# Kernel tuning notes

Hardware: AMD Instinct MI355X
Metric: run time of the kernel (lower is better)

The kernel has to match this reference:

```python
import jax, jax.numpy as jnp
import numpy as np

VOCAB, VEC, HID, ATT, DOM, B, S = 50000, 300, 256, 500, 16, 64, 128


def _gru_scan(gi_all, h0, Whh, bhh):
    # gi_all: [S,B,3H] precomputed input projections; returns hs: [S,B,H]
    def step(h, gi):
        gh = h @ Whh.T + bhh
        i_r, i_z, i_n = jnp.split(gi, 3, axis=-1)
        h_r, h_z, h_n = jnp.split(gh, 3, axis=-1)
        r = jax.nn.sigmoid(i_r + h_r)
        zg = jax.nn.sigmoid(i_z + h_z)
        n = jnp.tanh(i_n + r * h_n)
        h_new = (1.0 - zg) * n + zg * h
        return h_new, h_new
    _, hs = jax.lax.scan(step, h0, gi_all)
    return hs


def setup_inputs() -> dict:
    key = jax.random.key(0)
    ks = jax.random.split(key, 16)
    def xavier(k, shape):
        fan_in, fan_out = shape[-1], shape[0]
        std = float(np.sqrt(2.0 / (fan_in + fan_out)))
        return jax.random.normal(k, shape, dtype=jnp.float32) * std
    inp = {
        'x': jax.random.randint(ks[0], (B, S), 0, VOCAB),
        'z': jax.random.randint(ks[1], (B,), 0, DOM),
        'emb': jax.random.normal(ks[2], (VOCAB, VEC), dtype=jnp.float32) * 0.1,
        'Wih_f': xavier(ks[3], (3 * HID, VEC)),
        'Whh_f': xavier(ks[4], (3 * HID, HID)),
        'bih_f': jnp.zeros((3 * HID,), jnp.float32),
        'bhh_f': jnp.zeros((3 * HID,), jnp.float32),
        'Wih_b': xavier(ks[5], (3 * HID, VEC)),
        'Whh_b': xavier(ks[6], (3 * HID, HID)),
        'bih_b': jnp.zeros((3 * HID,), jnp.float32),
        'bhh_b': jnp.zeros((3 * HID,), jnp.float32),
        'att_fc_W': xavier(ks[7], (ATT, 2 * HID)),
        'att_fc_b': jnp.zeros((ATT,), jnp.float32),
        'att_weight': xavier(ks[8], (DOM, ATT)),
        'fc_W': xavier(ks[9], (2, 2 * HID)),
        'fc_b': jnp.zeros((2,), jnp.float32),
    }
    return inp


def reference(x, z, emb, Wih_f, Whh_f, bih_f, bhh_f, Wih_b, Whh_b, bih_b, bhh_b,
              att_fc_W, att_fc_b, att_weight, fc_W, fc_b):
    xe = emb[x]                              # [B,S,VEC]
    xs = jnp.transpose(xe, (1, 0, 2))        # [S,B,VEC] (seq-major like torch GRU)
    h0 = jnp.zeros((x.shape[0], HID), jnp.float32)
    gi_f = jnp.einsum('sbv,gv->sbg', xs, Wih_f) + bih_f
    hs_f = _gru_scan(gi_f, h0, Whh_f, bhh_f)                       # [S,B,H]
    gi_b = jnp.einsum('sbv,gv->sbg', xs[::-1], Wih_b) + bih_b
    hs_b = _gru_scan(gi_b, h0, Whh_b, bhh_b)[::-1]                 # [S,B,H]
    h = jnp.transpose(jnp.concatenate([hs_f, hs_b], axis=-1), (1, 0, 2))  # [B,S,2H]
    hr = jnp.tanh(jnp.einsum('bsh,ah->bsa', h, att_fc_W) + att_fc_b)      # [B,S,ATT]
    # batched gather of per-domain attention vector, then per-row dot
    u = jnp.einsum('bsa,ba->bs', hr, att_weight[z])                        # [B,S]
    att = jax.nn.softmax(u, axis=1)                                        # [B,S]
    pooled = jnp.einsum('bsh,bs->bh', h, att)                              # [B,2H]
    # dropout is identity in eval mode
    return pooled @ fc_W.T + fc_b                                          # [B,2]
```

## Files before the change

kernel.cpp:

```cpp
#include <hip/hip_runtime.h>
#include <math.h>

#define VEC   300
#define HID   256
#define ATT   500
#define NB    64
#define NS    128
#define G3    768
#define GIC   1536
#define H2    512

typedef _Float16 half1;
typedef _Float16 h2_t  __attribute__((ext_vector_type(2)));
typedef _Float16 f16x8 __attribute__((ext_vector_type(8)));
typedef float    f32x4 __attribute__((ext_vector_type(4)));

struct __align__(16) H8 { h2_t a, b, c, d; };

#if __has_builtin(__builtin_amdgcn_exp2f)
#define EXP2F(x) __builtin_amdgcn_exp2f(x)
#else
#define EXP2F(x) exp2f(x)
#endif
#if __has_builtin(__builtin_amdgcn_rcpf)
#define RCPF(x) __builtin_amdgcn_rcpf(x)
#else
#define RCPF(x) (1.0f/(x))
#endif

__device__ __forceinline__ float sigm(float x){ return RCPF(1.f + EXP2F(-1.44269504f*x)); }
__device__ __forceinline__ float tanh_fast(float x){ return 1.f - 2.f*RCPF(1.f + EXP2F(2.88539008f*x)); }

#if __has_builtin(__builtin_amdgcn_fdot2)
#define FDOT(w,h,acc) __builtin_amdgcn_fdot2((w),(h),(acc),false)
#else
#define FDOT(w,h,acc) ((acc) + (float)(w).x*(float)(h).x + (float)(w).y*(float)(h).y)
#endif

__global__ __launch_bounds__(256) void k_prep(const float* __restrict__ Wf,
                       const float* __restrict__ Wb, h2_t* __restrict__ Wpk){
  int o = blockIdx.x*256 + threadIdx.x;
  int t = o & 1023;
  int rest = o >> 10;
  int j = rest % 3;
  int p = (rest/3) & 31;
  int dir = rest / 96;
  int u = t & 255, ks = t >> 8;
  const float* W = dir ? Wb : Wf;
  int k0 = ks*64 + 2*p;
  h2_t w;
  w.x = (half1)W[(j*HID+u)*HID + k0];
  w.y = (half1)W[(j*HID+u)*HID + k0 + 1];
  Wpk[o] = w;
}

__global__ __launch_bounds__(256) void k_prepA(const float* __restrict__ afW,
                       half1* __restrict__ afW16){
  int o = blockIdx.x*256 + threadIdx.x;
  int n = o >> 9, k = o & 511;
  afW16[o] = (half1)((n < ATT) ? afW[n*H2 + k] : 0.f);
}

__global__ __launch_bounds__(256)
__attribute__((amdgpu_waves_per_eu(4, 4)))
void k_gi_mfma(const int* __restrict__ x,
      const float* __restrict__ emb,
      const float* __restrict__ Wf, const float* __restrict__ Wb,
      const float* __restrict__ bf, const float* __restrict__ bb,
      float* __restrict__ gi){
  __shared__ half1 Al[128*40];
  __shared__ half1 Bl[128*40];
  __shared__ int   xi[128];
  const int t = threadIdx.x;
  const int row0 = blockIdx.x * 128;
  const int col0 = blockIdx.y * 128;
  if (t < 128) {
    int i = row0 + t; int s = i >> 6; int b = i & 63;
    xi[t] = x[b*NS + s];
  }
  __syncthreads();

  const int lane = t & 63, wid = t >> 6;
  const int wr = wid >> 1, wc = wid & 1;
  const int l15 = lane & 15, lk = lane >> 4;

  f32x4 acc[4][4];
#pragma unroll
  for (int i = 0; i < 4; ++i)
#pragma unroll
    for (int j = 0; j < 4; ++j) acc[i][j] = (f32x4){0.f,0.f,0.f,0.f};

  for (int ks = 0; ks < 10; ++ks) {
#pragma unroll
    for (int l = 0; l < 8; ++l) {
      int idx = l*256 + t;
      int row = idx >> 4;
      int kp  = idx & 15;
      int kk  = ks*32 + kp*2;
      h2_t va; va.x = (half1)0.f; va.y = (half1)0.f;
      h2_t vb; vb.x = (half1)0.f; vb.y = (half1)0.f;
      if (kk < VEC) {
        float2 e = *reinterpret_cast<const float2*>(&emb[(long)xi[row]*VEC + kk]);
        va.x = (half1)e.x; va.y = (half1)e.y;
        int g = col0 + row;
        const float* W = (g < G3) ? &Wf[(long)g*VEC] : &Wb[(long)(g-G3)*VEC];
        float2 w2 = *reinterpret_cast<const float2*>(&W[kk]);
        vb.x = (half1)w2.x; vb.y = (half1)w2.y;
      }
      *reinterpret_cast<h2_t*>(&Al[row*40 + kp*2]) = va;
      *reinterpret_cast<h2_t*>(&Bl[row*40 + kp*2]) = vb;
    }
    __syncthreads();
    f16x8 af[4], bfq[4];
#pragma unroll
    for (int i = 0; i < 4; ++i)
      af[i]  = *reinterpret_cast<const f16x8*>(&Al[(wr*64 + i*16 + l15)*40 + lk*8]);
#pragma unroll
    for (int j = 0; j < 4; ++j)
      bfq[j] = *reinterpret_cast<const f16x8*>(&Bl[(wc*64 + j*16 + l15)*40 + lk*8]);
#pragma unroll
    for (int i = 0; i < 4; ++i)
#pragma unroll
      for (int j = 0; j < 4; ++j)
        acc[i][j] = __builtin_amdgcn_mfma_f32_16x16x32_f16(af[i], bfq[j], acc[i][j], 0, 0, 0);
    __syncthreads();
  }

#pragma unroll
  for (int j = 0; j < 4; ++j) {
    int gcol = col0 + wc*64 + j*16 + l15;
    float bj = (gcol < G3) ? bf[gcol] : bb[gcol - G3];
#pragma unroll
    for (int i = 0; i < 4; ++i) {
      int grow0 = row0 + wr*64 + i*16 + lk*4;
#pragma unroll
      for (int q = 0; q < 4; ++q)
        gi[(long)(grow0 + q)*GIC + gcol] = acc[i][j][q] + bj;
    }
  }
}

#define DECL12(X,g,UNUSED) h2_t X##g##a0,X##g##a1,X##g##a2, X##g##b0,X##g##b1,X##g##b2, \
                                X##g##c0,X##g##c1,X##g##c2, X##g##d0,X##g##d1,X##g##d2;
#define LOAD12(X,g,WP) \
  X##g##a0=(WP)[((4*(g)+0)*3+0)*1024]; X##g##a1=(WP)[((4*(g)+0)*3+1)*1024]; X##g##a2=(WP)[((4*(g)+0)*3+2)*1024]; \
  X##g##b0=(WP)[((4*(g)+1)*3+0)*1024]; X##g##b1=(WP)[((4*(g)+1)*3+1)*1024]; X##g##b2=(WP)[((4*(g)+1)*3+2)*1024]; \
  X##g##c0=(WP)[((4*(g)+2)*3+0)*1024]; X##g##c1=(WP)[((4*(g)+2)*3+1)*1024]; X##g##c2=(WP)[((4*(g)+2)*3+2)*1024]; \
  X##g##d0=(WP)[((4*(g)+3)*3+0)*1024]; X##g##d1=(WP)[((4*(g)+3)*3+1)*1024]; X##g##d2=(WP)[((4*(g)+3)*3+2)*1024];
#define FMA12(X,g,BOFF) { \
  H8 hv = *reinterpret_cast<const H8*>(&hl16[kb + (BOFF) + (g)*8]); \
  a0=FDOT(X##g##a0,hv.a,a0); a1=FDOT(X##g##a1,hv.a,a1); a2=FDOT(X##g##a2,hv.a,a2); \
  a0=FDOT(X##g##b0,hv.b,a0); a1=FDOT(X##g##b1,hv.b,a1); a2=FDOT(X##g##b2,hv.b,a2); \
  a0=FDOT(X##g##c0,hv.c,a0); a1=FDOT(X##g##c1,hv.c,a1); a2=FDOT(X##g##c2,hv.c,a2); \
  a0=FDOT(X##g##d0,hv.d,a0); a1=FDOT(X##g##d1,hv.d,a1); a2=FDOT(X##g##d2,hv.d,a2); }
#define GRP8(M,X,A2) M(X,0,A2) M(X,1,A2) M(X,2,A2) M(X,3,A2) M(X,4,A2) M(X,5,A2) M(X,6,A2) M(X,7,A2)

__global__ __launch_bounds__(512)
__attribute__((amdgpu_waves_per_eu(2, 2)))
void k_scan_reg2(const float* __restrict__ gi,
     const h2_t* __restrict__ Wpk,
     const float* __restrict__ bhf, const float* __restrict__ bhb,
     float* __restrict__ hseq){
  __shared__ __align__(16) half1 hl16[264];
  __shared__ float part[3*256];
  const int t   = threadIdx.x;
  const int u   = t & 255;
  const int ks  = t >> 8;
  const int kb  = ks * 128;
  const int dir = blockIdx.x & 1;
  const int b   = blockIdx.x >> 1;
  const float* bhh = dir ? bhb : bhf;
  const h2_t* wpA = Wpk + (long)dir*96*1024 + (2*ks)*256 + u;
  const h2_t* wpB = Wpk + (long)dir*96*1024 + (2*ks+1)*256 + u;

  GRP8(DECL12, A, 0)
  GRP8(DECL12, B, 0)
  GRP8(LOAD12, A, wpA)
  GRP8(LOAD12, B, wpB)

  float bh0=0.f, bh1=0.f, bh2=0.f;
  if (ks == 0) { bh0 = bhh[u]; bh1 = bhh[HID+u]; bh2 = bhh[2*HID+u]; }
  if (t < 256) hl16[t] = (half1)0.f;
  float hprev = 0.f;
  __syncthreads();

#pragma unroll 1
  for (int tt = 0; tt < NS; ++tt) {
    const int s = dir ? (NS-1-tt) : tt;
    float i0=0.f, i1=0.f, i2=0.f;
    if (ks == 0) {
      long base = ((long)s*NB + b)*GIC + dir*G3 + u;
      i0 = gi[base]; i1 = gi[base+HID]; i2 = gi[base+2*HID];
    }
    float a0=0.f, a1=0.f, a2=0.f;
    GRP8(FMA12, A, 0)
    GRP8(FMA12, B, 64)
    if (ks == 1) { part[u] = a0; part[256+u] = a1; part[512+u] = a2; }
    __syncthreads();
    if (ks == 0) {
      float g0 = bh0 + a0 + part[u];
      float g1 = bh1 + a1 + part[256+u];
      float g2 = bh2 + a2 + part[512+u];
      float r  = sigm(i0 + g0);
      float zg = sigm(i1 + g1);
      float n  = tanh_fast(i2 + r*g2);
      float hn = (1.f - zg)*n + zg*hprev;
      hprev = hn;
      hl16[u] = (half1)hn;
      hseq[((long)b*NS + s)*H2 + dir*HID + u] = hn;
    }
    __syncthreads();
  }
}

__global__ __launch_bounds__(256)
__attribute__((amdgpu_waves_per_eu(4, 4)))
void k_att1_mfma(const float* __restrict__ hseq, const half1* __restrict__ afW16,
    const float* __restrict__ afb, const float* __restrict__ attw,
    const int* __restrict__ z, float* __restrict__ ub){
  __shared__ half1 Ah[32*520];
  __shared__ float red[4*32];
  const int t  = threadIdx.x;
  const int b  = blockIdx.x;
  const int s0 = blockIdx.y * 32;
  const int lane = t & 63, w = t >> 6;
  const int l15 = lane & 15, lk = lane >> 4;

#pragma unroll
  for (int l = 0; l < 64; ++l) {
    int idx = l*256 + t;
    int sl = idx >> 9, c = idx & 511;
    Ah[sl*520 + c] = (half1)hseq[((long)b*NS + s0 + sl)*H2 + c];
  }
  __syncthreads();

  f32x4 acc[2][8];
#pragma unroll
  for (int i = 0; i < 2; ++i)
#pragma unroll
    for (int j = 0; j < 8; ++j) acc[i][j] = (f32x4){0.f,0.f,0.f,0.f};

#pragma unroll 2
  for (int ksn = 0; ksn < 16; ++ksn) {
    f16x8 af[2];
#pragma unroll
    for (int mt = 0; mt < 2; ++mt)
      af[mt] = *reinterpret_cast<const f16x8*>(&Ah[(mt*16 + l15)*520 + ksn*32 + lk*8]);
#pragma unroll
    for (int nt = 0; nt < 8; ++nt) {
      int n = w*128 + nt*16 + l15;
      f16x8 bf = *reinterpret_cast<const f16x8*>(&afW16[(long)n*512 + ksn*32 + lk*8]);
#pragma unroll
      for (int mt = 0; mt < 2; ++mt)
        acc[mt][nt] = __builtin_amdgcn_mfma_f32_16x16x32_f16(af[mt], bf, acc[mt][nt], 0, 0, 0);
    }
  }

  float us[8];
#pragma unroll
  for (int i = 0; i < 8; ++i) us[i] = 0.f;
  const int zb = z[b];
#pragma unroll
  for (int nt = 0; nt < 8; ++nt) {
    int n = w*128 + nt*16 + l15;
    float ab = (n < ATT) ? afb[n] : 0.f;
    float aw = (n < ATT) ? attw[zb*ATT + n] : 0.f;
#pragma unroll
    for (int mt = 0; mt < 2; ++mt)
#pragma unroll
      for (int q = 0; q < 4; ++q)
        us[mt*4+q] += tanh_fast(acc[mt][nt][q] + ab) * aw;
  }
#pragma unroll
  for (int off = 1; off < 16; off <<= 1)
#pragma unroll
    for (int i = 0; i < 8; ++i) us[i] += __shfl_xor(us[i], off, 64);
  if (l15 == 0) {
#pragma unroll
    for (int i = 0; i < 8; ++i) {
      int row = (i >> 2)*16 + lk*4 + (i & 3);
      red[w*32 + row] = us[i];
    }
  }
  __syncthreads();
  if (t < 32)
    ub[b*NS + s0 + t] = red[t] + red[32+t] + red[64+t] + red[96+t];
}

__global__ __launch_bounds__(256) void k_att2(const float* __restrict__ hseq,
   const float* __restrict__ ub, const float* __restrict__ fcW,
   const float* __restrict__ fcb, float* __restrict__ out){
  __shared__ float att[NS];
  __shared__ float red[256];
  __shared__ float pool[H2];
  const int t = threadIdx.x, b = blockIdx.x;
  float v = (t < NS) ? ub[b*NS + t] : -3.4e38f;
  red[t] = v; __syncthreads();
  for (int off = 128; off >= 1; off >>= 1) {
    if (t < off) red[t] = fmaxf(red[t], red[t+off]);
    __syncthreads();
  }
  float mx = red[0]; __syncthreads();
  float e = (t < NS) ? EXP2F(1.44269504f*(v - mx)) : 0.f;
  red[t] = e; __syncthreads();
  for (int off = 128; off >= 1; off >>= 1) {
    if (t < off) red[t] += red[t+off];
    __syncthreads();
  }
  float sm = red[0]; __syncthreads();
  if (t < NS) att[t] = e / sm;
  __syncthreads();
#pragma unroll
  for (int rep = 0; rep < 2; ++rep) {
    int c = rep*256 + t;
    float acc = 0.f;
#pragma unroll 4
    for (int s = 0; s < NS; ++s) acc += att[s] * hseq[((long)b*NS + s)*H2 + c];
    pool[c] = acc;
  }
  __syncthreads();
  for (int j = 0; j < 2; ++j) {
    float p = pool[t]*fcW[j*H2+t] + pool[t+256]*fcW[j*H2+t+256];
    red[t] = p; __syncthreads();
    for (int off = 128; off >= 1; off >>= 1) {
      if (t < off) red[t] += red[t+off];
      __syncthreads();
    }
    if (t == 0) out[b*2+j] = red[0] + fcb[j];
    __syncthreads();
  }
}

extern "C" void kernel_launch(void* const* d_in, const int* in_sizes, int n_in,
                              void* d_out, int out_size, void* d_ws, size_t ws_size,
                              hipStream_t stream) {
  const int*   x     = (const int*)  d_in[0];
  const int*   z     = (const int*)  d_in[1];
  const float* emb   = (const float*)d_in[2];
  const float* Wih_f = (const float*)d_in[3];
  const float* Whh_f = (const float*)d_in[4];
  const float* bih_f = (const float*)d_in[5];
  const float* bhh_f = (const float*)d_in[6];
  const float* Wih_b = (const float*)d_in[7];
  const float* Whh_b = (const float*)d_in[8];
  const float* bih_b = (const float*)d_in[9];
  const float* bhh_b = (const float*)d_in[10];
  const float* afW   = (const float*)d_in[11];
  const float* afb   = (const float*)d_in[12];
  const float* attw  = (const float*)d_in[13];
  const float* fcW   = (const float*)d_in[14];
  const float* fcb   = (const float*)d_in[15];

  float* ws    = (float*)d_ws;
  h2_t*  Wpk   = (h2_t*)ws;
  half1* afW16 = (half1*)(ws + 196608);
  float* giW   = ws   + 196608 + 131072;
  float* hseq  = giW  + 12582912;
  float* ubuf  = hseq + 4194304;

  k_prep <<<dim3(768),  dim3(256), 0, stream>>>(Whh_f, Whh_b, Wpk);
  k_prepA<<<dim3(1024), dim3(256), 0, stream>>>(afW, afW16);
  k_gi_mfma<<<dim3(64,12), dim3(256), 0, stream>>>(x, emb, Wih_f, Wih_b, bih_f, bih_b, giW);
  k_scan_reg2<<<dim3(128), dim3(512), 0, stream>>>(giW, Wpk, bhh_f, bhh_b, hseq);
  k_att1_mfma<<<dim3(64,4), dim3(256), 0, stream>>>(hseq, afW16, afb, attw, z, ubuf);
  k_att2<<<dim3(64), dim3(256), 0, stream>>>(hseq, ubuf, fcW, fcb, (float*)d_out);
}
```

Before: 233.8 us.

## Split GRU recurrent matvec across four K-slices with 1024-thread blocks

```diff
diff --git a/kernel.cpp b/kernel.cpp
--- a/kernel.cpp
+++ b/kernel.cpp
@@ -155,60 +155,63 @@
   a0=FDOT(X##g##d0,hv.d,a0); a1=FDOT(X##g##d1,hv.d,a1); a2=FDOT(X##g##d2,hv.d,a2); }
 #define GRP8(M,X,A2) M(X,0,A2) M(X,1,A2) M(X,2,A2) M(X,3,A2) M(X,4,A2) M(X,5,A2) M(X,6,A2) M(X,7,A2)
 
-__global__ __launch_bounds__(512)
-__attribute__((amdgpu_waves_per_eu(2, 2)))
-void k_scan_reg2(const float* __restrict__ gi,
+__global__ __launch_bounds__(1024)
+__attribute__((amdgpu_waves_per_eu(4, 4)))
+void k_scan_reg3(const float* __restrict__ gi,
      const h2_t* __restrict__ Wpk,
      const float* __restrict__ bhf, const float* __restrict__ bhb,
      float* __restrict__ hseq){
   __shared__ __align__(16) half1 hl16[264];
-  __shared__ float part[3*256];
+  __shared__ float part[3*780];
   const int t   = threadIdx.x;
   const int u   = t & 255;
   const int ks  = t >> 8;
-  const int kb  = ks * 128;
+  const int kb  = ks * 64;
   const int dir = blockIdx.x & 1;
   const int b   = blockIdx.x >> 1;
   const float* bhh = dir ? bhb : bhf;
-  const h2_t* wpA = Wpk + (long)dir*96*1024 + (2*ks)*256 + u;
-  const h2_t* wpB = Wpk + (long)dir*96*1024 + (2*ks+1)*256 + u;
+  const h2_t* wp = Wpk + (long)dir*96*1024 + t;
 
   GRP8(DECL12, A, 0)
-  GRP8(DECL12, B, 0)
-  GRP8(LOAD12, A, wpA)
-  GRP8(LOAD12, B, wpB)
+  GRP8(LOAD12, A, wp)
 
   float bh0=0.f, bh1=0.f, bh2=0.f;
   if (ks == 0) { bh0 = bhh[u]; bh1 = bhh[HID+u]; bh2 = bhh[2*HID+u]; }
   if (t < 256) hl16[t] = (half1)0.f;
   float hprev = 0.f;
+
+  const long gstep = dir ? -(long)NB*GIC : (long)NB*GIC;
+  const long hstep = dir ? -(long)H2    : (long)H2;
+  long gbase = ((long)(dir ? (NS-1) : 0)*NB + b)*GIC + dir*G3 + u;
+  long hbase = ((long)b*NS + (dir ? (NS-1) : 0))*H2 + dir*HID + u;
   __syncthreads();
 
 #pragma unroll 1
   for (int tt = 0; tt < NS; ++tt) {
-    const int s = dir ? (NS-1-tt) : tt;
     float i0=0.f, i1=0.f, i2=0.f;
     if (ks == 0) {
-      long base = ((long)s*NB + b)*GIC + dir*G3 + u;
-      i0 = gi[base]; i1 = gi[base+HID]; i2 = gi[base+2*HID];
+      i0 = gi[gbase]; i1 = gi[gbase+HID]; i2 = gi[gbase+2*HID];
     }
     float a0=0.f, a1=0.f, a2=0.f;
     GRP8(FMA12, A, 0)
-    GRP8(FMA12, B, 64)
-    if (ks == 1) { part[u] = a0; part[256+u] = a1; part[512+u] = a2; }
+    if (ks > 0) {
+      float* p = &part[(ks-1)*780 + u];
+      p[0] = a0; p[260] = a1; p[520] = a2;
+    }
     __syncthreads();
     if (ks == 0) {
-      float g0 = bh0 + a0 + part[u];
-      float g1 = bh1 + a1 + part[256+u];
-      float g2 = bh2 + a2 + part[512+u];
+      float g0 = bh0 + a0 + part[u]     + part[780+u]     + part[1560+u];
+      float g1 = bh1 + a1 + part[260+u] + part[1040+u]    + part[1820+u];
+      float g2 = bh2 + a2 + part[520+u] + part[1300+u]    + part[2080+u];
       float r  = sigm(i0 + g0);
       float zg = sigm(i1 + g1);
       float n  = tanh_fast(i2 + r*g2);
       float hn = (1.f - zg)*n + zg*hprev;
       hprev = hn;
       hl16[u] = (half1)hn;
-      hseq[((long)b*NS + s)*H2 + dir*HID + u] = hn;
-    }
+      hseq[hbase] = hn;
+    }
+    gbase += gstep; hbase += hstep;
     __syncthreads();
   }
 }
@@ -361,7 +364,7 @@
   k_prep <<<dim3(768),  dim3(256), 0, stream>>>(Whh_f, Whh_b, Wpk);
   k_prepA<<<dim3(1024), dim3(256), 0, stream>>>(afW, afW16);
   k_gi_mfma<<<dim3(64,12), dim3(256), 0, stream>>>(x, emb, Wih_f, Wih_b, bih_f, bih_b, giW);
-  k_scan_reg2<<<dim3(128), dim3(512), 0, stream>>>(giW, Wpk, bhh_f, bhh_b, hseq);
+  k_scan_reg3<<<dim3(128), dim3(1024), 0, stream>>>(giW, Wpk, bhh_f, bhh_b, hseq);
   k_att1_mfma<<<dim3(64,4), dim3(256), 0, stream>>>(hseq, afW16, afb, attw, z, ubuf);
   k_att2<<<dim3(64), dim3(256), 0, stream>>>(hseq, ubuf, fcW, fcb, (float*)d_out);
 }
```

Result: slower. 249.3 us (+6.6%).
